# Performance work log

Measured on AMD Instinct MI355X. Metric: run time of the kernel, lower is better.

The kernel has to match this reference:

```python
import jax, jax.numpy as jnp
import numpy as np

NUM_CLASS = 1000
FEAT_DIM = 512
BATCH = 131072


def _safe_cdist(a, b):
    # Euclidean distance matrix, numerically safe sqrt (0 on the diagonal,
    # finite gradient), matching torch.cdist(p=2).
    a2 = jnp.sum(a * a, axis=-1, keepdims=True)        # [Na, 1]
    b2 = jnp.sum(b * b, axis=-1)                       # [Nb]
    d2 = jnp.maximum(a2 + b2 - 2.0 * (a @ b.T), 0.0)   # [Na, Nb]
    pos = d2 > 0
    return jnp.where(pos, jnp.sqrt(jnp.where(pos, d2, 1.0)), 0.0)


def setup_inputs() -> dict:
    key = jax.random.key(0)
    kf, kl, kc = jax.random.split(key, 3)
    features = jax.random.normal(kf, (BATCH, FEAT_DIM), dtype=jnp.float32)
    labels = jax.random.randint(kl, (BATCH,), 0, NUM_CLASS)
    center = jax.random.normal(kc, (NUM_CLASS, FEAT_DIM), dtype=jnp.float32)
    return {"features": features, "center": center, "labels": labels}


def reference(features, center, labels):
    # Threshold computed from the initial centers in __init__ (detached).
    init_dist = _safe_cdist(center, center)                     # [C, C]
    thres_inter = jax.lax.stop_gradient(jnp.mean(init_dist)) * 3.0

    # Per-class accumulation: the Python loops in the torch code are exactly
    # a segment-sum (scatter-add) of features into centers + a bincount.
    counts = jax.ops.segment_sum(
        jnp.ones((labels.shape[0],), dtype=features.dtype), labels,
        num_segments=NUM_CLASS)                                  # [C]
    sums = jax.ops.segment_sum(features, labels, num_segments=NUM_CLASS)  # [C, D]
    new_center = (center + sums) / jnp.maximum(counts, 1.0)[:, None]

    dist = _safe_cdist(new_center, new_center)                   # [C, C]
    hinge = jnp.where(dist < thres_inter, thres_inter - dist, 0.0)
    inter_loss = jnp.mean(hinge)
    # torch forward returns (inter_loss, self.center.data) -- center was
    # mutated in place, so it is the updated per-class mean center.
    return (inter_loss, new_center)
```

## Files before the change

### kernel.cpp

```cpp
#include <hip/hip_runtime.h>
#include <hip/hip_bf16.h>
#include <math.h>

#define BATCH   131072
#define NCLASS  1000
#define FDIM    512
#define NTILE   136

typedef __attribute__((ext_vector_type(4))) float f32x4;
typedef __attribute__((ext_vector_type(8))) short short8;

#define OFF_COUNTS   0
#define OFF_CURSOR   4096
#define OFF_ACCS     8192
#define OFF_DONE     8200
#define OFF_GOFFS    12288
#define OFF_PERM     16384
#define OFF_PBUF     544768
#define OFF_WSM      8740864
static_assert(OFF_PERM + BATCH * 4 <= OFF_PBUF, "perm/pbuf overlap");
static_assert(OFF_PBUF + 4 * NCLASS * FDIM * 4 <= OFF_WSM, "pbuf/wsM overlap");
static_assert(OFF_GOFFS + 4096 <= OFF_PERM, "goffs/perm overlap");

__device__ __forceinline__ ushort f2bf(float x) {
    union { float f; unsigned u; } v; v.f = x;
    unsigned r = v.u + 0x7fff + ((v.u >> 16) & 1);
    return (ushort)(r >> 16);
}

template <int MODE>
__device__ void dist_mfma(const float* __restrict__ M, float th, int by, int bx,
                          float* __restrict__ accs) {
    __shared__ ushort Abf[64][72];
    __shared__ ushort Bbf[64][72];
    __shared__ float  rnA[64];
    __shared__ float  rnB[64];
    __shared__ float  red[256];

    const int tid  = threadIdx.x;
    const int lane = tid & 63;
    const int w    = tid >> 6;
    const int wr   = w >> 1, wc = w & 1;
    const int row4 = tid >> 2;
    const int cq   = tid & 3;
    const int gi_s = by * 64 + row4;
    const int gj_s = bx * 64 + row4;

    f32x4 acc[2][2];
#pragma unroll
    for (int m = 0; m < 2; ++m)
#pragma unroll
        for (int n = 0; n < 2; ++n) acc[m][n] = (f32x4){0.f, 0.f, 0.f, 0.f};

    float nA = 0.f, nB = 0.f;
    for (int k0 = 0; k0 < 8; ++k0) {
        __syncthreads();
#pragma unroll
        for (int c = 0; c < 4; ++c) {
            const int col  = cq * 16 + c * 4;
            const int gcol = k0 * 64 + col;
            f32x4 av = (f32x4){0.f, 0.f, 0.f, 0.f};
            f32x4 bv = (f32x4){0.f, 0.f, 0.f, 0.f};
            if (gi_s < NCLASS) av = *(const f32x4*)&M[(size_t)gi_s * FDIM + gcol];
            if (gj_s < NCLASS) bv = *(const f32x4*)&M[(size_t)gj_s * FDIM + gcol];
            nA += av.x * av.x + av.y * av.y + av.z * av.z + av.w * av.w;
            nB += bv.x * bv.x + bv.y * bv.y + bv.z * bv.z + bv.w * bv.w;
            ushort4 ap, bp;
            ap.x = f2bf(av.x); ap.y = f2bf(av.y); ap.z = f2bf(av.z); ap.w = f2bf(av.w);
            bp.x = f2bf(bv.x); bp.y = f2bf(bv.y); bp.z = f2bf(bv.z); bp.w = f2bf(bv.w);
            *(ushort4*)&Abf[row4][col] = ap;
            *(ushort4*)&Bbf[row4][col] = bp;
        }
        __syncthreads();
#pragma unroll
        for (int kk = 0; kk < 2; ++kk) {
            short8 a[2], b[2];
#pragma unroll
            for (int m = 0; m < 2; ++m)
                a[m] = *(const short8*)&Abf[wr * 32 + m * 16 + (lane & 15)]
                                          [kk * 32 + (lane >> 4) * 8];
#pragma unroll
            for (int n = 0; n < 2; ++n)
                b[n] = *(const short8*)&Bbf[wc * 32 + n * 16 + (lane & 15)]
                                          [kk * 32 + (lane >> 4) * 8];
#pragma unroll
            for (int m = 0; m < 2; ++m)
#pragma unroll
                for (int n = 0; n < 2; ++n)
                    acc[m][n] = __builtin_amdgcn_mfma_f32_16x16x32_bf16(
                        a[m], b[n], acc[m][n], 0, 0, 0);
        }
    }

    nA += __shfl_xor(nA, 1, 64); nA += __shfl_xor(nA, 2, 64);
    nB += __shfl_xor(nB, 1, 64); nB += __shfl_xor(nB, 2, 64);
    if (cq == 0) { rnA[row4] = nA; rnB[row4] = nB; }
    __syncthreads();

    float local = 0.f;
#pragma unroll
    for (int m = 0; m < 2; ++m)
#pragma unroll
        for (int n = 0; n < 2; ++n)
#pragma unroll
            for (int i = 0; i < 4; ++i) {
                const int r_l = wr * 32 + m * 16 + (lane >> 4) * 4 + i;
                const int c_l = wc * 32 + n * 16 + (lane & 15);
                const int gi = by * 64 + r_l;
                const int gj = bx * 64 + c_l;
                if (gi < NCLASS && gj < NCLASS && gj > gi) {
                    float d2 = rnA[r_l] + rnB[c_l] - 2.0f * acc[m][n][i];
                    d2 = fmaxf(d2, 0.0f);
                    float dst = (d2 > 0.0f) ? sqrtf(d2) : 0.0f;
                    if (MODE == 1) {
                        if (dst < th) local += th - dst;
                    } else {
                        local += dst;
                    }
                }
            }

    red[tid] = local;
    __syncthreads();
    for (int s = 128; s > 0; s >>= 1) {
        if (tid < s) red[tid] += red[tid + s];
        __syncthreads();
    }
    if (tid == 0) atomicAdd(&accs[MODE], red[0]);
}

__global__ __launch_bounds__(256)
void k2_hist_scan_scatter_dist0(const int* __restrict__ labels,
                                int* __restrict__ cursor0,
                                int* __restrict__ perm,
                                int* __restrict__ g_offsets,
                                int* __restrict__ g_counts,
                                const float* __restrict__ center,
                                float* __restrict__ accs) {
    const int b = blockIdx.x, t = threadIdx.x;
    __shared__ int sH[1024];
    __shared__ int sB[1024];

    if (b >= BATCH / 1024) {
        int idx = b - BATCH / 1024;
        int by = 0;
        while (idx >= 16 - by) { idx -= 16 - by; ++by; }
        dist_mfma<0>(center, 0.0f, by, by + idx, accs);
        return;
    }

    for (int i = t; i < 1024; i += 256) sH[i] = 0;
    __syncthreads();
    const int4* l4 = (const int4*)labels;
    for (int i = t; i < BATCH / 4; i += 256) {
        int4 l = l4[i];
        atomicAdd(&sH[l.x], 1);
        atomicAdd(&sH[l.y], 1);
        atomicAdd(&sH[l.z], 1);
        atomicAdd(&sH[l.w], 1);
    }
    __syncthreads();
    if (b == 0)
        for (int i = t; i < 1024; i += 256) g_counts[i] = sH[i];

    int* cur = sH;
    int* nxt = sB;
    for (int off = 1; off < 1024; off <<= 1) {
        for (int i = t; i < 1024; i += 256) {
            int v = cur[i];
            if (i >= off) v += cur[i - off];
            nxt[i] = v;
        }
        __syncthreads();
        int* tmp = cur; cur = nxt; nxt = tmp;
    }
    int* offp = nxt;
    for (int i = t; i < 1024; i += 256) offp[i] = i ? cur[i - 1] : 0;
    __syncthreads();
    if (b == 0)
        for (int i = t; i < 1024; i += 256) g_offsets[i] = offp[i];

    const int gid = b * 256 + t;
    int4 l = l4[gid];
    const int r = gid * 4;
    perm[offp[l.x] + atomicAdd(&cursor0[l.x], 1)] = r + 0;
    perm[offp[l.y] + atomicAdd(&cursor0[l.y], 1)] = r + 1;
    perm[offp[l.z] + atomicAdd(&cursor0[l.z], 1)] = r + 2;
    perm[offp[l.w] + atomicAdd(&cursor0[l.w], 1)] = r + 3;
}

__global__ __launch_bounds__(256)
void k3_gather(const float* __restrict__ features,
               const int* __restrict__ g_offsets,
               const int* __restrict__ counts,
               const int* __restrict__ perm,
               float* __restrict__ pbuf) {
    const int c = blockIdx.x, q = blockIdx.y, t = threadIdx.x;
    const int half = t >> 7;
    const int pos  = t & 127;
    const int beg = g_offsets[c], n = counts[c];
    const int per = (n + 1) >> 1;
    const int s0  = q * per;
    const int e0  = min(n, s0 + per);
    const int cnt = e0 - s0;
    const int* pp = perm + beg + s0;

    f32x4 acc = (f32x4){0.f, 0.f, 0.f, 0.f};
    int idx[8];
    int r = half;
    if (r + 14 < cnt) {
#pragma unroll
        for (int u = 0; u < 8; ++u) idx[u] = pp[r + 2 * u];
    }
    while (r + 14 < cnt) {
        const int nr = r + 16;
        int nidx[8];
        if (nr + 14 < cnt) {
#pragma unroll
            for (int u = 0; u < 8; ++u) nidx[u] = pp[nr + 2 * u];
        } else {
#pragma unroll
            for (int u = 0; u < 8; ++u) nidx[u] = 0;
        }
        f32x4 v0 = *(const f32x4*)&features[(size_t)idx[0] * FDIM + pos * 4];
        f32x4 v1 = *(const f32x4*)&features[(size_t)idx[1] * FDIM + pos * 4];
        f32x4 v2 = *(const f32x4*)&features[(size_t)idx[2] * FDIM + pos * 4];
        f32x4 v3 = *(const f32x4*)&features[(size_t)idx[3] * FDIM + pos * 4];
        f32x4 v4 = *(const f32x4*)&features[(size_t)idx[4] * FDIM + pos * 4];
        f32x4 v5 = *(const f32x4*)&features[(size_t)idx[5] * FDIM + pos * 4];
        f32x4 v6 = *(const f32x4*)&features[(size_t)idx[6] * FDIM + pos * 4];
        f32x4 v7 = *(const f32x4*)&features[(size_t)idx[7] * FDIM + pos * 4];
        acc += ((v0 + v1) + (v2 + v3)) + ((v4 + v5) + (v6 + v7));
#pragma unroll
        for (int u = 0; u < 8; ++u) idx[u] = nidx[u];
        r = nr;
    }
    for (; r < cnt; r += 2) {
        acc += *(const f32x4*)&features[(size_t)pp[r] * FDIM + pos * 4];
    }
    const int slot = q * 2 + half;
    *(f32x4*)&pbuf[((size_t)slot * NCLASS + c) * FDIM + pos * 4] = acc;
}

__global__ __launch_bounds__(128)
void k4_finalize(const float* __restrict__ center,
                 const float* __restrict__ pbuf,
                 const int* __restrict__ counts,
                 float* __restrict__ out_center,
                 float* __restrict__ wsM) {
    const int c = blockIdx.x, t = threadIdx.x;
    f32x4 s = (f32x4){0.f, 0.f, 0.f, 0.f};
#pragma unroll
    for (int slot = 0; slot < 4; ++slot)
        s += *(const f32x4*)&pbuf[((size_t)slot * NCLASS + c) * FDIM + t * 4];
    f32x4 cc = *(const f32x4*)&center[(size_t)c * FDIM + t * 4];
    const float invn = 1.0f / fmaxf((float)counts[c], 1.0f);
    f32x4 nc = (cc + s) * invn;
    float* o = out_center + (size_t)c * FDIM + t * 4;
    o[0] = nc.x; o[1] = nc.y; o[2] = nc.z; o[3] = nc.w;
    *(f32x4*)&wsM[(size_t)c * FDIM + t * 4] = nc;
}

__global__ __launch_bounds__(256)
void k5_dist1(const float* __restrict__ wsM, float* __restrict__ accs,
              int* __restrict__ done, float* __restrict__ out0) {
    int idx = blockIdx.x;
    int by = 0;
    while (idx >= 16 - by) { idx -= 16 - by; ++by; }
    const float th = 6.0f * accs[0] * 1e-6f;
    dist_mfma<1>(wsM, th, by, by + idx, accs);
    if (threadIdx.x == 0) {
        __threadfence();
        if (atomicAdd(done, 1) == NTILE - 1) {
            __threadfence();
            const float l1 = atomicAdd(&accs[1], 0.0f);
            const double thd = 6.0 * (double)accs[0] * 1e-6;
            out0[0] = (float)((2.0 * (double)l1 + (double)NCLASS * thd) * 1e-6);
        }
    }
}

extern "C" void kernel_launch(void* const* d_in, const int* in_sizes, int n_in,
                              void* d_out, int out_size, void* d_ws, size_t ws_size,
                              hipStream_t stream) {
    const float* features = (const float*)d_in[0];
    const float* center   = (const float*)d_in[1];
    const int*   labels   = (const int*)d_in[2];
    float* out = (float*)d_out;
    char*  ws  = (char*)d_ws;

    int*   counts    = (int*)(ws + OFF_COUNTS);
    int*   cursor0   = (int*)(ws + OFF_CURSOR);
    float* accs      = (float*)(ws + OFF_ACCS);
    int*   done      = (int*)(ws + OFF_DONE);
    int*   g_offsets = (int*)(ws + OFF_GOFFS);
    int*   perm      = (int*)(ws + OFF_PERM);
    float* pbuf      = (float*)(ws + OFF_PBUF);
    float* wsM       = (float*)(ws + OFF_WSM);

    hipMemsetAsync(ws, 0, 8208, stream);
    k2_hist_scan_scatter_dist0<<<BATCH / 1024 + NTILE, 256, 0, stream>>>(
        labels, cursor0, perm, g_offsets, counts, center, accs);
    k3_gather<<<dim3(NCLASS, 2), 256, 0, stream>>>(features, g_offsets, counts,
                                                   perm, pbuf);
    k4_finalize<<<NCLASS, 128, 0, stream>>>(center, pbuf, counts, out + 1, wsM);
    k5_dist1<<<NTILE, 256, 0, stream>>>(wsM, accs, done, out);
}
```

Baseline: 145.7 us.

## Fuse gather and finalize into one 512-thread block per class

Merges the per-class gather kernel and the finalize kernel into one launch. Each class now gets a single 512-thread block whose four row-strided partial sums are reduced in shared memory before the new center is written. This removes the global partial-sum buffer round trip and one kernel launch. In exchange there are half as many blocks (1000 instead of 2000), which could lower occupancy and latency hiding for the memory-bound gather.

```diff
diff --git a/kernel.cpp b/kernel.cpp
--- a/kernel.cpp
+++ b/kernel.cpp
@@ -16,11 +16,9 @@
 #define OFF_DONE     8200
 #define OFF_GOFFS    12288
 #define OFF_PERM     16384
-#define OFF_PBUF     544768
-#define OFF_WSM      8740864
-static_assert(OFF_PERM + BATCH * 4 <= OFF_PBUF, "perm/pbuf overlap");
-static_assert(OFF_PBUF + 4 * NCLASS * FDIM * 4 <= OFF_WSM, "pbuf/wsM overlap");
+#define OFF_WSM      540672
 static_assert(OFF_GOFFS + 4096 <= OFF_PERM, "goffs/perm overlap");
+static_assert(OFF_PERM + BATCH * 4 <= OFF_WSM, "perm/wsM overlap");
 
 __device__ __forceinline__ ushort f2bf(float x) {
     union { float f; unsigned u; } v; v.f = x;
@@ -189,35 +187,34 @@
     perm[offp[l.w] + atomicAdd(&cursor0[l.w], 1)] = r + 3;
 }
 
-__global__ __launch_bounds__(256)
-void k3_gather(const float* __restrict__ features,
-               const int* __restrict__ g_offsets,
-               const int* __restrict__ counts,
-               const int* __restrict__ perm,
-               float* __restrict__ pbuf) {
-    const int c = blockIdx.x, q = blockIdx.y, t = threadIdx.x;
-    const int half = t >> 7;
-    const int pos  = t & 127;
-    const int beg = g_offsets[c], n = counts[c];
-    const int per = (n + 1) >> 1;
-    const int s0  = q * per;
-    const int e0  = min(n, s0 + per);
-    const int cnt = e0 - s0;
-    const int* pp = perm + beg + s0;
+__global__ __launch_bounds__(512)
+void k3_gather_finalize(const float* __restrict__ features,
+                        const int* __restrict__ g_offsets,
+                        const int* __restrict__ counts,
+                        const int* __restrict__ perm,
+                        const float* __restrict__ center,
+                        float* __restrict__ out_center,
+                        float* __restrict__ wsM) {
+    const int c = blockIdx.x, t = threadIdx.x;
+    const int par = t >> 7;
+    const int pos = t & 127;
+    const int n   = counts[c];
+    const int* pp = perm + g_offsets[c];
+    __shared__ float part[4][128][4];
 
     f32x4 acc = (f32x4){0.f, 0.f, 0.f, 0.f};
     int idx[8];
-    int r = half;
-    if (r + 14 < cnt) {
-#pragma unroll
-        for (int u = 0; u < 8; ++u) idx[u] = pp[r + 2 * u];
-    }
-    while (r + 14 < cnt) {
-        const int nr = r + 16;
+    int r = par;
+    if (r + 28 < n) {
+#pragma unroll
+        for (int u = 0; u < 8; ++u) idx[u] = pp[r + 4 * u];
+    }
+    while (r + 28 < n) {
+        const int nr = r + 32;
         int nidx[8];
-        if (nr + 14 < cnt) {
-#pragma unroll
-            for (int u = 0; u < 8; ++u) nidx[u] = pp[nr + 2 * u];
+        if (nr + 28 < n) {
+#pragma unroll
+            for (int u = 0; u < 8; ++u) nidx[u] = pp[nr + 4 * u];
         } else {
 #pragma unroll
             for (int u = 0; u < 8; ++u) nidx[u] = 0;
@@ -235,30 +232,23 @@
         for (int u = 0; u < 8; ++u) idx[u] = nidx[u];
         r = nr;
     }
-    for (; r < cnt; r += 2) {
+    for (; r < n; r += 4)
         acc += *(const f32x4*)&features[(size_t)pp[r] * FDIM + pos * 4];
-    }
-    const int slot = q * 2 + half;
-    *(f32x4*)&pbuf[((size_t)slot * NCLASS + c) * FDIM + pos * 4] = acc;
-}
-
-__global__ __launch_bounds__(128)
-void k4_finalize(const float* __restrict__ center,
-                 const float* __restrict__ pbuf,
-                 const int* __restrict__ counts,
-                 float* __restrict__ out_center,
-                 float* __restrict__ wsM) {
-    const int c = blockIdx.x, t = threadIdx.x;
-    f32x4 s = (f32x4){0.f, 0.f, 0.f, 0.f};
-#pragma unroll
-    for (int slot = 0; slot < 4; ++slot)
-        s += *(const f32x4*)&pbuf[((size_t)slot * NCLASS + c) * FDIM + t * 4];
-    f32x4 cc = *(const f32x4*)&center[(size_t)c * FDIM + t * 4];
-    const float invn = 1.0f / fmaxf((float)counts[c], 1.0f);
-    f32x4 nc = (cc + s) * invn;
-    float* o = out_center + (size_t)c * FDIM + t * 4;
-    o[0] = nc.x; o[1] = nc.y; o[2] = nc.z; o[3] = nc.w;
-    *(f32x4*)&wsM[(size_t)c * FDIM + t * 4] = nc;
+
+    *(f32x4*)&part[par][pos][0] = acc;
+    __syncthreads();
+    if (t < 128) {
+        f32x4 s = *(const f32x4*)&part[0][t][0];
+        s += *(const f32x4*)&part[1][t][0];
+        s += *(const f32x4*)&part[2][t][0];
+        s += *(const f32x4*)&part[3][t][0];
+        const f32x4 cc = *(const f32x4*)&center[(size_t)c * FDIM + t * 4];
+        const float invn = 1.0f / fmaxf((float)n, 1.0f);
+        const f32x4 nc = (cc + s) * invn;
+        float* o = out_center + (size_t)c * FDIM + t * 4;
+        o[0] = nc.x; o[1] = nc.y; o[2] = nc.z; o[3] = nc.w;
+        *(f32x4*)&wsM[(size_t)c * FDIM + t * 4] = nc;
+    }
 }
 
 __global__ __launch_bounds__(256)
@@ -295,14 +285,12 @@
     int*   done      = (int*)(ws + OFF_DONE);
     int*   g_offsets = (int*)(ws + OFF_GOFFS);
     int*   perm      = (int*)(ws + OFF_PERM);
-    float* pbuf      = (float*)(ws + OFF_PBUF);
     float* wsM       = (float*)(ws + OFF_WSM);
 
     hipMemsetAsync(ws, 0, 8208, stream);
     k2_hist_scan_scatter_dist0<<<BATCH / 1024 + NTILE, 256, 0, stream>>>(
         labels, cursor0, perm, g_offsets, counts, center, accs);
-    k3_gather<<<dim3(NCLASS, 2), 256, 0, stream>>>(features, g_offsets, counts,
-                                                   perm, pbuf);
-    k4_finalize<<<NCLASS, 128, 0, stream>>>(center, pbuf, counts, out + 1, wsM);
+    k3_gather_finalize<<<NCLASS, 512, 0, stream>>>(features, g_offsets, counts,
+                                                   perm, center, out + 1, wsM);
     k5_dist1<<<NTILE, 256, 0, stream>>>(wsM, accs, done, out);
 }
```

Result: faster. 141.5 us (-2.9%).
